# Optimization experiments

Measured on AMD Instinct MI355X. Metric: run time of the kernel, lower is better.

## Reference

```python
import jax, jax.numpy as jnp
import numpy as np

B, L, D, H = 8, 512, 512, 8  # d_keys = d_values = d_model = D (default path)


def setup_inputs() -> dict:
    key = jax.random.key(0)
    ks = jax.random.split(key, 9)
    w = 0.02
    return {
        "queries": jax.random.normal(ks[0], (B, L, D), dtype=jnp.float32),
        "keys": jax.random.normal(ks[1], (B, L, D), dtype=jnp.float32),
        "values": jax.random.normal(ks[2], (B, L, D), dtype=jnp.float32),
        "Wq": jax.random.normal(ks[3], (D, D * H), dtype=jnp.float32) * w,
        "bq": jnp.zeros((D * H,), dtype=jnp.float32),
        "Wk": jax.random.normal(ks[4], (D, D * H), dtype=jnp.float32) * w,
        "bk": jnp.zeros((D * H,), dtype=jnp.float32),
        "Wv": jax.random.normal(ks[5], (D, D * H), dtype=jnp.float32) * w,
        "bv": jnp.zeros((D * H,), dtype=jnp.float32),
        "attn_mask": 0,  # must be falsy; original code would crash on a real tensor mask
    }


def reference(queries, keys, values, Wq, bq, Wk, bk, Wv, bv, attn_mask):
    b, l, d = queries.shape
    h = Wq.shape[1] // d
    # projections -> (B, L, H, E) with E = d_model
    q = (queries @ Wq + bq).reshape(b, l, h, d)
    k = (keys @ Wk + bk).reshape(b, l, h, d)
    v = (values @ Wv + bv).reshape(b, l, h, d)
    scale = 1.0 / np.sqrt(d).astype(np.float32)
    # per-position head-vs-head scores (B, L, H, H); equivalent to the i-loop
    s = jnp.einsum('blhe,blge->blhg', q, k) * scale
    p = jax.nn.softmax(s, axis=-1)
    # diagonal (l == i) contribution, summed over positions -> (B, H, E)
    attn_part = jnp.einsum('blhg,blge->bhe', p, v)
    # off-diagonal (l != i): uniform 1/H softmax of zero scores, (L-1) copies
    uniform_part = (jnp.float32(l - 1) / h) * v.sum(axis=(1, 2))  # (B, E)
    out = attn_part + uniform_part[:, None, :]  # (B, H, E)
    # final view(B, L, -1): requires L | H*E
    return out.reshape(b, l, -1)
```

## Files before the change

### kernel.cpp

```cpp
#include <hip/hip_runtime.h>


using f32x4 = __attribute__((ext_vector_type(4))) float;

#define GLOAD16(gp, lp) __builtin_amdgcn_global_load_lds( \
    (const __attribute__((address_space(1))) unsigned int*)(gp), \
    (__attribute__((address_space(3))) unsigned int*)(lp), 16, 0, 0)

__global__ __launch_bounds__(256) void prep(
    const float* __restrict__ x0, const float* __restrict__ x1,
    unsigned char* __restrict__ o0, unsigned char* __restrict__ o1,
    const float* __restrict__ w0, const float* __restrict__ w1,
    unsigned char* __restrict__ t0, unsigned char* __restrict__ t1)
{
    const int z = blockIdx.z;
    if (z < 2) {
        const float* src = (z == 0) ? x0 : x1;
        unsigned char* dst = (z == 0) ? o0 : o1;
        int i = (blockIdx.x * 256 + threadIdx.x) * 4;
        float4 a = *(const float4*)(src + i);
        unsigned int u = __builtin_amdgcn_cvt_pk_fp8_f32(a.x, a.y, 0u, false);
        u = __builtin_amdgcn_cvt_pk_fp8_f32(a.z, a.w, u, true);
        *(unsigned int*)(dst + i) = u;
    } else {
        if (blockIdx.x >= 512) return;
        const float* W = (z == 2) ? w0 : w1;
        unsigned char* T = (z == 2) ? t0 : t1;
        __shared__ float tile[64][67];
        const int kt = blockIdx.x >> 6, nt = blockIdx.x & 63;
        const int k0 = kt * 64, n0 = nt * 64;
        const int tid = threadIdx.x;
        #pragma unroll
        for (int it = 0; it < 4; ++it) {
            int f = it * 256 + tid;
            int r = f >> 4, c4 = f & 15;
            float4 v = *(const float4*)(W + (size_t)(k0 + r) * 4096 + n0 + c4 * 4);
            tile[r][c4 * 4 + 0] = v.x; tile[r][c4 * 4 + 1] = v.y;
            tile[r][c4 * 4 + 2] = v.z; tile[r][c4 * 4 + 3] = v.w;
        }
        __syncthreads();
        const int n = tid >> 2, kq = tid & 3;
        unsigned int pk4[4];
        #pragma unroll
        for (int q = 0; q < 4; ++q) {
            const int kk = kq * 16 + q * 4;
            unsigned int pk = __builtin_amdgcn_cvt_pk_fp8_f32(
                16.f * tile[kk + 0][n], 16.f * tile[kk + 1][n], 0u, false);
            pk = __builtin_amdgcn_cvt_pk_fp8_f32(
                16.f * tile[kk + 2][n], 16.f * tile[kk + 3][n], pk, true);
            pk4[q] = pk;
        }
        *(uint4*)(T + (size_t)(n0 + n) * 512 + k0 + kq * 16) =
            make_uint4(pk4[0], pk4[1], pk4[2], pk4[3]);
    }
}

__global__ __launch_bounds__(512) void gemm_bt256(
    const unsigned char* __restrict__ a0, const unsigned char* __restrict__ a1,
    const unsigned char* __restrict__ w0, const unsigned char* __restrict__ w1,
    const float* __restrict__ b0, const float* __restrict__ b1,
    unsigned char* __restrict__ c0, unsigned char* __restrict__ c1)
{
    const unsigned char* A;  const unsigned char* Bt; const float* bias; unsigned char* C;
    if (blockIdx.z == 0) { A = a0; Bt = w0; bias = b0; C = c0; }
    else                 { A = a1; Bt = w1; bias = b1; C = c1; }

    __shared__ __align__(16) unsigned char SH[65536];

    const int tid  = threadIdx.x;
    const int lane = tid & 63;
    const int wid  = tid >> 6;
    const int wr   = wid >> 2;
    const int wn   = wid & 3;
    const int linb = blockIdx.y * 16 + blockIdx.x;
    const int swz  = (linb & 7) * 32 + (linb >> 3);
    const int bx   = (swz >> 6) * 4 + (swz & 3);
    const int by   = (swz >> 2) & 15;
    const int row0 = by * 256;
    const int n0   = bx * 256;

    const int lgs = (tid & 7) ^ ((tid >> 3) & 7);
    const int shi = lgs >> 2, slo = lgs & 3;
    const int srow0 = (tid >> 3) + shi * 128;
    const unsigned char* gA = A  + (size_t)(row0 + srow0) * 512 + slo * 16;
    const unsigned char* gB = Bt + (size_t)(n0   + srow0) * 512 + slo * 16;

#define STAGE_A(gp, buf, c, trel)                                                 \
    GLOAD16((gp) + (c) * (64 * 512) + (trel) * 64,                                \
            SH + (buf) * 16384 + (c) * 8192 + wid * 1024)
#define STAGE_B(gp, buf, c, trel)                                                 \
    GLOAD16((gp) + (c) * (64 * 512) + (trel) * 64,                                \
            SH + 32768 + (buf) * 16384 + (c) * 8192 + wid * 1024)

    const int l7 = lane & 7, koh = lane >> 5, kol = (lane >> 4) & 1, l15 = lane & 15;
    const char* bA0 = (const char*)SH + l15 * 128 + (((0 * 2 + koh + wr * 4) ^ l7) << 4) + kol * 8;
    const char* bA1 = (const char*)SH + l15 * 128 + (((1 * 2 + koh + wr * 4) ^ l7) << 4) + kol * 8;
    const char* bB0 = (const char*)SH + 32768 + (wn & 1) * 8192 + l15 * 128
                      + (((0 * 2 + koh + (wn >> 1) * 4) ^ l7) << 4) + kol * 8;
    const char* bB1 = (const char*)SH + 32768 + (wn & 1) * 8192 + l15 * 128
                      + (((1 * 2 + koh + (wn >> 1) * 4) ^ l7) << 4) + kol * 8;

#define LD_A(c, m, s) (*(const long long*)(((s) ? bA1 : bA0) + (c) * 16384 + (m) * 2048))
#define LD_B(c, n, s) (*(const long long*)(((s) ? bB1 : bB0) + (c) * 16384 + (n) * 2048))

#define BAR() __builtin_amdgcn_s_barrier()
#define VMC2() asm volatile("s_waitcnt vmcnt(2)" ::: "memory")
#define VMC0() asm volatile("s_waitcnt vmcnt(0)" ::: "memory")

    f32x4 acc[8][4];
    #pragma unroll
    for (int m = 0; m < 8; ++m)
        #pragma unroll
        for (int n = 0; n < 4; ++n)
            acc[m][n] = (f32x4){0.f, 0.f, 0.f, 0.f};

    long long bfr[4][2];
    long long fa0, fa1, fa2, fa3, fa4, fa5, fa6, fa7;

#define LDA_H(c, h) { fa0 = LD_A(c, 4*(h)+0, 0); fa1 = LD_A(c, 4*(h)+0, 1);       \
                      fa2 = LD_A(c, 4*(h)+1, 0); fa3 = LD_A(c, 4*(h)+1, 1);       \
                      fa4 = LD_A(c, 4*(h)+2, 0); fa5 = LD_A(c, 4*(h)+2, 1);       \
                      fa6 = LD_A(c, 4*(h)+3, 0); fa7 = LD_A(c, 4*(h)+3, 1); }
#define LDB_ALL(c) { _Pragma("unroll") for (int n = 0; n < 4; ++n) {              \
                       bfr[n][0] = LD_B(c, n, 0); bfr[n][1] = LD_B(c, n, 1); } }
#define MFMA_H(h) {                                                               \
    _Pragma("unroll") for (int n = 0; n < 4; ++n) {                               \
      acc[4*(h)+0][n] = __builtin_amdgcn_mfma_f32_16x16x32_fp8_fp8(bfr[n][0], fa0, acc[4*(h)+0][n], 0,0,0); \
      acc[4*(h)+0][n] = __builtin_amdgcn_mfma_f32_16x16x32_fp8_fp8(bfr[n][1], fa1, acc[4*(h)+0][n], 0,0,0); \
      acc[4*(h)+1][n] = __builtin_amdgcn_mfma_f32_16x16x32_fp8_fp8(bfr[n][0], fa2, acc[4*(h)+1][n], 0,0,0); \
      acc[4*(h)+1][n] = __builtin_amdgcn_mfma_f32_16x16x32_fp8_fp8(bfr[n][1], fa3, acc[4*(h)+1][n], 0,0,0); \
      acc[4*(h)+2][n] = __builtin_amdgcn_mfma_f32_16x16x32_fp8_fp8(bfr[n][0], fa4, acc[4*(h)+2][n], 0,0,0); \
      acc[4*(h)+2][n] = __builtin_amdgcn_mfma_f32_16x16x32_fp8_fp8(bfr[n][1], fa5, acc[4*(h)+2][n], 0,0,0); \
      acc[4*(h)+3][n] = __builtin_amdgcn_mfma_f32_16x16x32_fp8_fp8(bfr[n][0], fa6, acc[4*(h)+3][n], 0,0,0); \
      acc[4*(h)+3][n] = __builtin_amdgcn_mfma_f32_16x16x32_fp8_fp8(bfr[n][1], fa7, acc[4*(h)+3][n], 0,0,0); } }

    STAGE_B(gB, 0, 0, 0); STAGE_B(gB, 0, 1, 0);
    STAGE_A(gA, 0, 0, 0); STAGE_A(gA, 0, 1, 0);
    STAGE_B(gB, 1, 0, 1); STAGE_B(gB, 1, 1, 1);
    VMC2();
    BAR();

    const unsigned char* gAt = gA;
    const unsigned char* gBt = gB;
    for (int i = 0; i < 4; ++i) {
        const bool s23 = (i < 3);

        LDA_H(0, 0); LDB_ALL(0);
        STAGE_A(gAt, 1, 0, 1); STAGE_A(gAt, 1, 1, 1);
        BAR(); MFMA_H(0); BAR();

        LDA_H(0, 1);
        if (s23) { STAGE_B(gBt, 0, 0, 2); STAGE_B(gBt, 0, 1, 2); }
        BAR(); MFMA_H(1);
        if (s23) { VMC2(); } else { VMC0(); }
        BAR();

        LDA_H(1, 0); LDB_ALL(1);
        if (s23) { STAGE_A(gAt, 0, 0, 2); STAGE_A(gAt, 0, 1, 2); }
        BAR(); MFMA_H(0); BAR();

        LDA_H(1, 1);
        if (s23) { STAGE_B(gBt, 1, 0, 3); STAGE_B(gBt, 1, 1, 3); }
        BAR(); MFMA_H(1);
        if (s23) { VMC2(); }
        BAR();

        gAt += 128; gBt += 128;
    }

    {
        const int q  = lane >> 4;
        const int tr = wr * 128 + (lane & 15);
        #pragma unroll
        for (int n = 0; n < 4; ++n) {
            float4 bb = *(const float4*)(bias + n0 + wn * 64 + n * 16 + q * 4);
            const int g16 = wn * 4 + n;
            #pragma unroll
            for (int m = 0; m < 8; ++m) {
                const int trm = tr + m * 16;
                unsigned int pk = __builtin_amdgcn_cvt_pk_fp8_f32(
                    acc[m][n][0] + 16.f * bb.x, acc[m][n][1] + 16.f * bb.y, 0u, false);
                pk = __builtin_amdgcn_cvt_pk_fp8_f32(
                    acc[m][n][2] + 16.f * bb.z, acc[m][n][3] + 16.f * bb.w, pk, true);
                *(unsigned int*)(SH + trm * 256 + ((g16 ^ (trm & 15)) << 4) + q * 4) = pk;
            }
        }
        BAR();
        #pragma unroll
        for (int it = 0; it < 8; ++it) {
            const int f = it * 512 + tid;
            const int rr = f >> 4, gg = f & 15;
            uint4 v = *(const uint4*)(SH + rr * 256 + ((gg ^ (rr & 15)) << 4));
            *(uint4*)(C + (size_t)(row0 + rr) * 4096 + gg * 16 + n0) = v;
        }
    }
#undef STAGE_A
#undef STAGE_B
#undef LD_A
#undef LD_B
}

__global__ __launch_bounds__(256) void mfscores(const unsigned char* __restrict__ Q,
                                                const unsigned char* __restrict__ K,
                                                float* __restrict__ P,
                                                float* __restrict__ pbpart)
{
    __shared__ __align__(16) unsigned char Qs[32768];
    __shared__ __align__(16) unsigned char Ks[32768];
    __shared__ float Pl[8 * 64];
    const int b = blockIdx.x, lc = blockIdx.y;
    const int tid = threadIdx.x, lane = tid & 63, w = tid >> 6;
    const int l0 = lc * 8;

    {
        const unsigned char* Qg = Q + (size_t)(b * 512 + l0) * 4096;
        const unsigned char* Kg = K + (size_t)(b * 512 + l0) * 4096;
        const int hhs = tid >> 5;
        const int dst = hhs * 512 + (((tid & 31) ^ hhs) << 4);
        #pragma unroll
        for (int i = 0; i < 8; ++i) {
            *(uint4*)(Qs + i * 4096 + dst) = *(const uint4*)(Qg + i * 4096 + tid * 16);
            *(uint4*)(Ks + i * 4096 + dst) = *(const uint4*)(Kg + i * 4096 + tid * 16);
        }
    }
    __syncthreads();

    const int colr = lane & 15;
    const int ko   = lane >> 4;
    const int lrow = w * 2 + (colr >> 3);
    const int hh   = colr & 7;
    const unsigned char* qb = Qs + lrow * 4096 + hh * 512 + (ko & 1) * 8;
    const unsigned char* kb = Ks + lrow * 4096 + hh * 512 + (ko & 1) * 8;
    const int koh = ko >> 1;

    f32x4 acc0 = (f32x4){0.f, 0.f, 0.f, 0.f};
    f32x4 acc1 = (f32x4){0.f, 0.f, 0.f, 0.f};
    #pragma unroll
    for (int kt = 0; kt < 8; ++kt) {
        const int s0 = (((2 * (2 * kt)     + koh) ^ hh) << 4);
        const int s1 = (((2 * (2 * kt + 1) + koh) ^ hh) << 4);
        long long a0 = *(const long long*)(qb + s0);
        long long b0 = *(const long long*)(kb + s0);
        long long a1 = *(const long long*)(qb + s1);
        long long b1 = *(const long long*)(kb + s1);
        acc0 = __builtin_amdgcn_mfma_f32_16x16x32_fp8_fp8(a0, b0, acc0, 0, 0, 0);
        acc1 = __builtin_amdgcn_mfma_f32_16x16x32_fp8_fp8(a1, b1, acc1, 0, 0, 0);
    }

    const int lpr = ko >> 1;
    const int lpc = (lane >> 3) & 1;
    #pragma unroll
    for (int r = 0; r < 4; ++r) {
        float s = (acc0[r] + acc1[r]) * 1.7263349150062e-4f;
        float m = s;
        m = fmaxf(m, __shfl_xor(m, 1));
        m = fmaxf(m, __shfl_xor(m, 2));
        m = fmaxf(m, __shfl_xor(m, 4));
        float e = __expf(s - m);
        float ss = e;
        ss += __shfl_xor(ss, 1);
        ss += __shfl_xor(ss, 2);
        ss += __shfl_xor(ss, 4);
        float p = e / ss + 63.875f;
        if (lpr == lpc)
            Pl[(w * 2 + lpr) * 64 + ((ko & 1) * 4 + r) * 8 + (lane & 7)] = p;
    }
    __syncthreads();

    {
        const int l = tid >> 5, off = (tid & 31) * 2;
        float2 v = *(const float2*)&Pl[l * 64 + off];
        *(float2*)(P + (size_t)(b * 512 + l0 + l) * 64 + off) = v;
    }
    if (tid < 64) {
        float s = 0.f;
        #pragma unroll
        for (int l = 0; l < 8; ++l) s += Pl[l * 64 + tid];
        pbpart[((size_t)b * 64 + lc) * 64 + tid] = s;
    }
}

__global__ __launch_bounds__(256) void ykern(const float* __restrict__ P,
                                             const float* __restrict__ Xv,
                                             float* __restrict__ ypart)
{
    __shared__ float Pl[128 * 64];
    __shared__ float Xl[128 * 64];
    const int b = blockIdx.x, dt = blockIdx.y, lc = blockIdx.z;
    const int tid = threadIdx.x;
    const int tm = tid & 15, te = tid >> 4;

    const float* Pg = P + ((size_t)b * 512 + lc * 128) * 64;
    #pragma unroll
    for (int i = 0; i < 8; ++i)
        *(float4*)&Pl[(i * 256 + tid) * 4] = *(const float4*)(Pg + (size_t)(i * 256 + tid) * 4);
    const float* Xg = Xv + ((size_t)b * 512 + lc * 128) * 512 + dt * 64;
    #pragma unroll
    for (int i = 0; i < 8; ++i) {
        int flat = i * 256 + tid;
        int r = flat >> 4, q = flat & 15;
        *(float4*)&Xl[r * 64 + q * 4] = *(const float4*)(Xg + (size_t)r * 512 + q * 4);
    }
    __syncthreads();

    float4 acc[4];
    #pragma unroll
    for (int i = 0; i < 4; ++i) acc[i] = make_float4(0.f, 0.f, 0.f, 0.f);

    for (int l = 0; l < 128; ++l) {
        float4 pv = *(const float4*)&Pl[l * 64 + tm * 4];
        float4 xv = *(const float4*)&Xl[l * 64 + te * 4];
        acc[0].x += pv.x * xv.x; acc[0].y += pv.x * xv.y; acc[0].z += pv.x * xv.z; acc[0].w += pv.x * xv.w;
        acc[1].x += pv.y * xv.x; acc[1].y += pv.y * xv.y; acc[1].z += pv.y * xv.z; acc[1].w += pv.y * xv.w;
        acc[2].x += pv.z * xv.x; acc[2].y += pv.z * xv.y; acc[2].z += pv.z * xv.z; acc[2].w += pv.z * xv.w;
        acc[3].x += pv.w * xv.x; acc[3].y += pv.w * xv.y; acc[3].z += pv.w * xv.z; acc[3].w += pv.w * xv.w;
    }
    #pragma unroll
    for (int i = 0; i < 4; ++i)
        *(float4*)&ypart[(((size_t)lc * 8 + b) * 64 + tm * 4 + i) * 512 + dt * 64 + te * 4] = acc[i];
}

__global__ __launch_bounds__(256) void vgemm(const float* __restrict__ ypart,
                                             const float* __restrict__ Wv,
                                             float* __restrict__ partial)
{
    __shared__ float Al[64 * 64];
    __shared__ float Bl[64 * 64];
    const int et = blockIdx.x, kc = blockIdx.y;
    const int g = kc >> 3, d0 = (kc & 7) * 64, e0 = et * 64;
    const int tid = threadIdx.x;
    const int tm = tid & 15, te = tid >> 4;

    #pragma unroll
    for (int i = 0; i < 4; ++i) {
        int flat = i * 256 + tid;
        int bh = flat >> 4, dq = flat & 15;
        int yrow = (bh >> 3) * 64 + (bh & 7) * 8 + g;
        size_t base = ((size_t)(yrow >> 6) * 64 + (yrow & 63)) * 512 + d0 + dq * 4;
        float4 v = *(const float4*)(ypart + base);
        #pragma unroll
        for (int lc = 1; lc < 4; ++lc) {
            float4 t = *(const float4*)(ypart + (size_t)lc * 262144 + base);
            v.x += t.x; v.y += t.y; v.z += t.z; v.w += t.w;
        }
        *(float4*)&Al[bh * 64 + ((dq ^ (bh >> 2)) << 2)] = v;
    }
    #pragma unroll
    for (int i = 0; i < 4; ++i) {
        int flat = i * 256 + tid;
        int kk = flat >> 4, eq = flat & 15;
        *(float4*)&Bl[kk * 64 + eq * 4] =
            *(const float4*)(Wv + (size_t)(d0 + kk) * 4096 + g * 512 + e0 + eq * 4);
    }
    __syncthreads();

    float4 acc[4];
    #pragma unroll
    for (int j = 0; j < 4; ++j) acc[j] = make_float4(0.f, 0.f, 0.f, 0.f);

    for (int k = 0; k < 64; ++k) {
        float4 b4 = *(const float4*)&Bl[k * 64 + te * 4];
        const int gcol = (((k >> 2) ^ tm) << 2) + (k & 3);
        #pragma unroll
        for (int j = 0; j < 4; ++j) {
            float a = Al[(tm * 4 + j) * 64 + gcol];
            acc[j].x += a * b4.x; acc[j].y += a * b4.y;
            acc[j].z += a * b4.z; acc[j].w += a * b4.w;
        }
    }
    #pragma unroll
    for (int j = 0; j < 4; ++j)
        *(float4*)&partial[(size_t)kc * 32768 + (tm * 4 + j) * 512 + e0 + te * 4] = acc[j];
}

__global__ __launch_bounds__(256) void finalize(const float* __restrict__ partial,
                                                const float* __restrict__ pbpart,
                                                const float* __restrict__ bv,
                                                float* __restrict__ out)
{
    __shared__ float red[64];
    __shared__ float csh[8];
    const int blk = blockIdx.x;
    const int tid = threadIdx.x;
    const int b = blk >> 4, h = (blk >> 1) & 7;
    const int e = (blk & 1) * 256 + tid;

    if (tid < 64) {
        const int g = tid >> 3, seg = tid & 7;
        float s = 0.f;
        #pragma unroll
        for (int j = 0; j < 8; ++j)
            s += pbpart[((size_t)b * 64 + seg * 8 + j) * 64 + h * 8 + g];
        red[tid] = s;
    }
    __syncthreads();
    if (tid < 8) {
        float s = 0.f;
        #pragma unroll
        for (int seg = 0; seg < 8; ++seg) s += red[tid + seg * 8];
        csh[tid] = s;
    }
    __syncthreads();

    const int i = ((b * 8 + h) << 9) + e;
    float s = 0.f;
    #pragma unroll
    for (int kc = 0; kc < 64; ++kc) s += partial[(size_t)kc * 32768 + i];
    float bt = 0.f;
    #pragma unroll
    for (int g = 0; g < 8; ++g) bt += csh[g] * bv[g * 512 + e];
    out[i] = s + bt;
}

extern "C" void kernel_launch(void* const* d_in, const int* in_sizes, int n_in,
                              void* d_out, int out_size, void* d_ws, size_t ws_size,
                              hipStream_t stream)
{
    const float* queries = (const float*)d_in[0];
    const float* keys    = (const float*)d_in[1];
    const float* values  = (const float*)d_in[2];
    const float* Wq      = (const float*)d_in[3];
    const float* bq      = (const float*)d_in[4];
    const float* Wk      = (const float*)d_in[5];
    const float* bk      = (const float*)d_in[6];
    const float* Wv      = (const float*)d_in[7];
    const float* bv      = (const float*)d_in[8];

    unsigned char* xq  = (unsigned char*)d_ws;
    unsigned char* xk  = xq  + (1u << 21);
    unsigned char* wtq = xk  + (1u << 21);
    unsigned char* wtk = wtq + (1u << 21);
    unsigned char* Q   = wtk + (1u << 21);
    unsigned char* Kb  = Q   + (1u << 24);
    float* P      = (float*)(Kb + (1u << 24));
    float* pbpart = P + 262144;
    float* ypart  = pbpart + 32768;
    float* part   = ypart + 4 * 262144;

    prep<<<dim3(2048, 1, 4), 256, 0, stream>>>(queries, keys, xq, xk, Wq, Wk, wtq, wtk);
    gemm_bt256<<<dim3(16, 16, 2), 512, 0, stream>>>(xq, xk, wtq, wtk, bq, bk, Q, Kb);
    mfscores<<<dim3(8, 64), 256, 0, stream>>>(Q, Kb, P, pbpart);
    ykern<<<dim3(8, 8, 4), 256, 0, stream>>>(P, values, ypart);
    vgemm<<<dim3(8, 64), 256, 0, stream>>>(ypart, Wv, part);
    finalize<<<dim3(128), 256, 0, stream>>>(part, pbpart, bv, (float*)d_out);
}
```

Baseline: 73.51 us.

## Restructure GEMM main loop into triple-buffered LDS pipeline with one barrier per stage

Replaces the double-buffered, four-barrier-per-iteration K loop in the fp8 projection GEMM with a fully unrolled 8-step loop over a three-slot LDS ring (96 KB). Each step issues async global-to-LDS loads two stages ahead, waits on vmcnt(4), and uses a single barrier plus explicit lgkmcnt waits and sched barriers around the MFMA halves. The goal is to cut barrier count and hide global latency further. In exchange it uses more shared memory, which can lower occupancy, and it pins the instruction schedule by hand.

After: 74.61 us. About the same (+1.5%).

```diff
diff --git a/kernel.cpp b/kernel.cpp
--- a/kernel.cpp
+++ b/kernel.cpp
@@ -65,7 +65,7 @@
     if (blockIdx.z == 0) { A = a0; Bt = w0; bias = b0; C = c0; }
     else                 { A = a1; Bt = w1; bias = b1; C = c1; }
 
-    __shared__ __align__(16) unsigned char SH[65536];
+    __shared__ __align__(16) unsigned char SH[98304];
 
     const int tid  = threadIdx.x;
     const int lane = tid & 63;
@@ -90,22 +90,24 @@
             SH + (buf) * 16384 + (c) * 8192 + wid * 1024)
 #define STAGE_B(gp, buf, c, trel)                                                 \
     GLOAD16((gp) + (c) * (64 * 512) + (trel) * 64,                                \
-            SH + 32768 + (buf) * 16384 + (c) * 8192 + wid * 1024)
+            SH + 49152 + (buf) * 16384 + (c) * 8192 + wid * 1024)
 
     const int l7 = lane & 7, koh = lane >> 5, kol = (lane >> 4) & 1, l15 = lane & 15;
     const char* bA0 = (const char*)SH + l15 * 128 + (((0 * 2 + koh + wr * 4) ^ l7) << 4) + kol * 8;
     const char* bA1 = (const char*)SH + l15 * 128 + (((1 * 2 + koh + wr * 4) ^ l7) << 4) + kol * 8;
-    const char* bB0 = (const char*)SH + 32768 + (wn & 1) * 8192 + l15 * 128
+    const char* bB0 = (const char*)SH + 49152 + (wn & 1) * 8192 + l15 * 128
                       + (((0 * 2 + koh + (wn >> 1) * 4) ^ l7) << 4) + kol * 8;
-    const char* bB1 = (const char*)SH + 32768 + (wn & 1) * 8192 + l15 * 128
+    const char* bB1 = (const char*)SH + 49152 + (wn & 1) * 8192 + l15 * 128
                       + (((1 * 2 + koh + (wn >> 1) * 4) ^ l7) << 4) + kol * 8;
 
 #define LD_A(c, m, s) (*(const long long*)(((s) ? bA1 : bA0) + (c) * 16384 + (m) * 2048))
 #define LD_B(c, n, s) (*(const long long*)(((s) ? bB1 : bB0) + (c) * 16384 + (n) * 2048))
 
 #define BAR() __builtin_amdgcn_s_barrier()
-#define VMC2() asm volatile("s_waitcnt vmcnt(2)" ::: "memory")
+#define VMC4() asm volatile("s_waitcnt vmcnt(4)" ::: "memory")
 #define VMC0() asm volatile("s_waitcnt vmcnt(0)" ::: "memory")
+#define LGKM0() asm volatile("s_waitcnt lgkmcnt(0)" ::: "memory")
+#define SCHB() __builtin_amdgcn_sched_barrier(0)
 
     f32x4 acc[8][4];
     #pragma unroll
@@ -134,39 +136,27 @@
       acc[4*(h)+3][n] = __builtin_amdgcn_mfma_f32_16x16x32_fp8_fp8(bfr[n][0], fa6, acc[4*(h)+3][n], 0,0,0); \
       acc[4*(h)+3][n] = __builtin_amdgcn_mfma_f32_16x16x32_fp8_fp8(bfr[n][1], fa7, acc[4*(h)+3][n], 0,0,0); } }
 
-    STAGE_B(gB, 0, 0, 0); STAGE_B(gB, 0, 1, 0);
-    STAGE_A(gA, 0, 0, 0); STAGE_A(gA, 0, 1, 0);
-    STAGE_B(gB, 1, 0, 1); STAGE_B(gB, 1, 1, 1);
-    VMC2();
+    STAGE_A(gA, 0, 0, 0); STAGE_A(gA, 0, 1, 0); STAGE_B(gB, 0, 0, 0); STAGE_B(gB, 0, 1, 0);
+    STAGE_A(gA, 1, 0, 1); STAGE_A(gA, 1, 1, 1); STAGE_B(gB, 1, 0, 1); STAGE_B(gB, 1, 1, 1);
+
+    #pragma unroll
+    for (int p = 0; p < 8; ++p) {
+        if (p < 7) { VMC4(); } else { VMC0(); }
+        BAR();
+        if (p < 6) {
+            const int sb = (p + 2) % 3;
+            STAGE_A(gA, sb, 0, p + 2); STAGE_A(gA, sb, 1, p + 2);
+            STAGE_B(gB, sb, 0, p + 2); STAGE_B(gB, sb, 1, p + 2);
+        }
+        const int cb = p % 3;
+        LDB_ALL(cb); LDA_H(cb, 0);
+        LGKM0(); SCHB();
+        MFMA_H(0);
+        LDA_H(cb, 1);
+        LGKM0(); SCHB();
+        MFMA_H(1);
+    }
     BAR();
-
-    const unsigned char* gAt = gA;
-    const unsigned char* gBt = gB;
-    for (int i = 0; i < 4; ++i) {
-        const bool s23 = (i < 3);
-
-        LDA_H(0, 0); LDB_ALL(0);
-        STAGE_A(gAt, 1, 0, 1); STAGE_A(gAt, 1, 1, 1);
-        BAR(); MFMA_H(0); BAR();
-
-        LDA_H(0, 1);
-        if (s23) { STAGE_B(gBt, 0, 0, 2); STAGE_B(gBt, 0, 1, 2); }
-        BAR(); MFMA_H(1);
-        if (s23) { VMC2(); } else { VMC0(); }
-        BAR();
-
-        LDA_H(1, 0); LDB_ALL(1);
-        if (s23) { STAGE_A(gAt, 0, 0, 2); STAGE_A(gAt, 0, 1, 2); }
-        BAR(); MFMA_H(0); BAR();
-
-        LDA_H(1, 1);
-        if (s23) { STAGE_B(gBt, 1, 0, 3); STAGE_B(gBt, 1, 1, 3); }
-        BAR(); MFMA_H(1);
-        if (s23) { VMC2(); }
-        BAR();
-
-        gAt += 128; gBt += 128;
-    }
 
     {
         const int q  = lane >> 4;
```
